# Kernel tuning notes

Hardware: AMD Instinct MI355X
Metric: run time of the kernel (lower is better)

The kernel has to match this reference:

```python
import jax, jax.numpy as jnp
import numpy as np

H = 128
W = 128
DELTA = 7000.0  # sigmainv in the original (delta default 7000)


def setup_inputs() -> dict:
    key = jax.random.key(0)
    k1, k2, k3, k4 = jax.random.split(key, 4)
    B, P, F, TH, TW = 2, 300, 512, 512, 512
    points_bxpx3 = jax.random.uniform(k1, (B, P, 3), jnp.float32) * 2.0 - 1.0  # NDC cube [-1,1]
    faces_fx3 = jax.random.randint(k2, (F, 3), 0, P, dtype=jnp.int32)
    uv_bxpx2 = jax.random.uniform(k3, (B, P, 2), jnp.float32)  # texcoords in [0,1]
    texture_bx3xthxtw = jax.random.uniform(k4, (B, 3, TH, TW), jnp.float32)
    return {"points_bxpx3": points_bxpx3, "faces_fx3": faces_fx3,
            "uv_bxpx2": uv_bxpx2, "texture_bx3xthxtw": texture_bx3xthxtw}


def _edge(ax, ay, bx, by, px, py):
    # signed area * 2 of triangle (a, b, p); standard edge function
    return (bx - ax) * (py - ay) - (by - ay) * (px - ax)


def _seg_d2(ax, ay, bx, by, px, py):
    # squared distance from point p to segment (a, b)
    abx, aby = bx - ax, by - ay
    apx, apy = px - ax, py - ay
    denom = abx * abx + aby * aby + 1e-12
    t = jnp.clip((apx * abx + apy * aby) / denom, 0.0, 1.0)
    dx = apx - t * abx
    dy = apy - t * aby
    return dx * dx + dy * dy


def _rasterize(points_bxpx3, faces_fx3, feats_bxfx3xd, height, width, delta):
    """Soft DIB-R-style rasterizer.
    Returns (imfeat [B,H,W,D], improb [B,H,W,1]).
    """
    B = points_bxpx3.shape[0]
    v = points_bxpx3[:, faces_fx3]                      # (B,F,3,3) gathered face vertices
    x0, x1, x2 = (v[:, :, i, 0][:, :, None, None] for i in range(3))
    y0, y1, y2 = (v[:, :, i, 1][:, :, None, None] for i in range(3))
    z0, z1, z2 = (v[:, :, i, 2][:, :, None, None] for i in range(3))

    # pixel-center grid in NDC; y flipped (top row = +1)
    px = ((jnp.arange(width, dtype=points_bxpx3.dtype) + 0.5) / width * 2.0 - 1.0)[None, None, None, :]
    py = (1.0 - (jnp.arange(height, dtype=points_bxpx3.dtype) + 0.5) / height * 2.0)[None, None, :, None]

    area = _edge(x0, y0, x1, y1, x2, y2)                # (B,F,1,1) == normal_z (cross-product z)
    front = area > 1e-8                                  # front-facing (normalz > 0) cull
    inv_area = 1.0 / jnp.where(front, area, 1.0)

    w0 = _edge(x1, y1, x2, y2, px, py) * inv_area        # (B,F,H,W) barycentrics
    w1 = _edge(x2, y2, x0, y0, px, py) * inv_area
    w2 = _edge(x0, y0, x1, y1, px, py) * inv_area
    inside = front & (w0 >= 0) & (w1 >= 0) & (w2 >= 0)

    z_pix = w0 * z0 + w1 * z1 + w2 * z2                  # interpolated depth
    zbuf = jnp.where(inside, z_pix, -1e9)
    best = jnp.argmax(zbuf, axis=1)                      # (B,H,W) nearest covering face
    hit = jnp.any(inside, axis=1)[..., None].astype(points_bxpx3.dtype)  # (B,H,W,1)

    # gather winning barycentrics and per-face vertex features
    w = jnp.stack([w0, w1, w2], axis=-1)                 # (B,F,H,W,3)
    idx = jnp.broadcast_to(best[:, None, :, :, None], (B, 1, height, width, 3))
    wb = jnp.take_along_axis(w, idx, axis=1)[:, 0]       # (B,H,W,3)
    fb = jax.vmap(lambda f, i: f[i])(feats_bxfx3xd, best)  # (B,H,W,3,D)
    imfeat = jnp.einsum('bhwk,bhwkd->bhwd', wb, fb) * hit

    # soft coverage: prob of each face = exp(-delta * d2(pixel, triangle)); z-buffer blend
    d2 = jnp.minimum(
        jnp.minimum(_seg_d2(x0, y0, x1, y1, px, py), _seg_d2(x1, y1, x2, y2, px, py)),
        _seg_d2(x2, y2, x0, y0, px, py))
    d2 = jnp.where(inside, 0.0, d2)
    p = jnp.where(front, jnp.exp(-delta * d2), 0.0)      # (B,F,H,W)
    log_miss = jnp.sum(jnp.log1p(-jnp.clip(p, 0.0, 1.0 - 1e-7)), axis=1)  # (B,H,W)
    improb = (1.0 - jnp.exp(log_miss))[..., None]
    return imfeat, improb


def _fragmentshader(imtexcoords, texture_bx3xthxtw, hardmask):
    # bilinear texture sampling; background is zero
    B, C, TH, TW = texture_bx3xthxtw.shape
    u = jnp.clip(imtexcoords[..., 0], 0.0, 1.0)
    vv = jnp.clip(imtexcoords[..., 1], 0.0, 1.0)
    fx = u * (TW - 1)
    fy = (1.0 - vv) * (TH - 1)
    x0 = jnp.floor(fx).astype(jnp.int32); x1 = jnp.minimum(x0 + 1, TW - 1)
    y0 = jnp.floor(fy).astype(jnp.int32); y1 = jnp.minimum(y0 + 1, TH - 1)
    wx = (fx - x0)[:, None]; wy = (fy - y0)[:, None]     # (B,1,H,W)

    def g(tex, yy, xx):  # tex (C,TH,TW), yy/xx (H,W) -> (C,H,W)
        return tex[:, yy, xx]
    c00 = jax.vmap(g)(texture_bx3xthxtw, y0, x0)
    c01 = jax.vmap(g)(texture_bx3xthxtw, y0, x1)
    c10 = jax.vmap(g)(texture_bx3xthxtw, y1, x0)
    c11 = jax.vmap(g)(texture_bx3xthxtw, y1, x1)
    col = (c00 * (1 - wx) * (1 - wy) + c01 * wx * (1 - wy)
           + c10 * (1 - wx) * wy + c11 * wx * wy)        # (B,C,H,W)
    return col.transpose(0, 2, 3, 1) * hardmask          # (B,H,W,C)


def reference(points_bxpx3, faces_fx3, uv_bxpx2, texture_bx3xthxtw):
    # texture mode: per-face vertex features = [u, v, mask=1]
    uvf = uv_bxpx2[:, faces_fx3]                          # (B,F,3,2)
    ones = jnp.ones_like(uvf[..., :1])
    feats = jnp.concatenate([uvf, ones], axis=-1)         # (B,F,3,3)
    imfeat, improb = _rasterize(points_bxpx3, faces_fx3, feats, H, W, DELTA)
    imtexcoords = imfeat[..., :2]
    hardmask = jax.lax.stop_gradient(imfeat[..., 2:3])    # .detach() in the original
    imrender = _fragmentshader(imtexcoords, texture_bx3xthxtw, hardmask)
    return imrender, improb
```

## Files before the change

kernel.cpp:

```cpp
#include <hip/hip_runtime.h>
#include <math.h>

constexpr int kB = 2, kP = 300, kF = 512, kH = 128, kW = 128, kTH = 512, kTW = 512;
constexpr float kDelta = 7000.0f;
constexpr float kCut = 0.06f;
constexpr float kThr2 = 0.018882f;
constexpr float kLogInside = -15.9423847f;

__global__ __launch_bounds__(512, 6) void render_all(const float* __restrict__ pts,
                                                     const int* __restrict__ faces,
                                                     const float* __restrict__ uvs,
                                                     const float* __restrict__ tex,
                                                     float* __restrict__ out) {
    __shared__ float4 sA[kF], sB[kF], sC[kF];
    __shared__ float2 s_vtx[kF * 3];
    __shared__ unsigned short s_of[kF];
    __shared__ int s_wsum[8];
    __shared__ float s_bz[512];
    __shared__ int s_bi[512];
    __shared__ float s_lm[512];

    int tile = (int)blockIdx.x;
    int b = tile >> 8;
    int rem = tile & 255;
    int ty = rem >> 4, tx = rem & 15;
    int tid = (int)threadIdx.x;
    int lane = tid & 63;
    int wv = tid >> 6;

    {
        int f = tid;
        int i0 = faces[f * 3 + 0], i1 = faces[f * 3 + 1], i2 = faces[f * 3 + 2];
        const float* pb = pts + b * kP * 3;
        float x0 = pb[i0 * 3], y0 = pb[i0 * 3 + 1], z0 = pb[i0 * 3 + 2];
        float x1 = pb[i1 * 3], y1 = pb[i1 * 3 + 1], z1 = pb[i1 * 3 + 2];
        float x2 = pb[i2 * 3], y2 = pb[i2 * 3 + 1], z2 = pb[i2 * 3 + 2];
        float area = (x1 - x0) * (y2 - y0) - (y1 - y0) * (x2 - x0);
        bool front = area > 1e-8f;

        sA[f] = make_float4(0.0f, 0.0f, -1e30f, 0.0f);
        sB[f] = make_float4(0.0f, -1e30f, 0.0f, 0.0f);
        sC[f] = make_float4(-1e30f, 0.0f, 0.0f, 0.0f);
        s_vtx[f * 3 + 0] = make_float2(1e15f, 1e15f);
        s_vtx[f * 3 + 1] = make_float2(1e15f, 1e15f);
        s_vtx[f * 3 + 2] = make_float2(1e15f, 1e15f);
        unsigned long long bal = __ballot(front);
        if (lane == 0) s_wsum[wv] = __popcll(bal);
        __syncthreads();

        int base = 0;
#pragma unroll
        for (int w = 0; w < 8; ++w) base += (w < wv) ? s_wsum[w] : 0;
        int k = base + __popcll(bal & ((1ull << lane) - 1ull));

        if (front) {
            int slot = ((k & 7) << 6) | (k >> 3);
            float inv_a = 1.0f / area;
            float e0x = x2 - x1, e0y = y2 - y1;
            float e1x = x0 - x2, e1y = y0 - y2;
            float e2x = x1 - x0, e2y = y1 - y0;
            float l0 = fmaf(e0x, e0x, e0y * e0y);
            float l1 = fmaf(e1x, e1x, e1y * e1y);
            float l2 = fmaf(e2x, e2x, e2y * e2y);
            float s0 = rsqrtf(l0 + 1e-12f);
            float s1 = rsqrtf(l1 + 1e-12f);
            float s2 = rsqrtf(l2 + 1e-12f);
            float A0 = -e0y * s0, B0 = e0x * s0, C0 = (e0y * x1 - e0x * y1) * s0;
            float A1 = -e1y * s1, B1 = e1x * s1, C1 = (e1y * x2 - e1x * y2) * s1;
            float A2 = -e2y * s2, B2 = e2x * s2, C2 = (e2y * x0 - e2x * y0) * s2;
            float a0 = -e0y * inv_a, b0 = e0x * inv_a, c0 = (e0y * x1 - e0x * y1) * inv_a;
            float a1 = -e1y * inv_a, b1 = e1x * inv_a, c1 = (e1y * x2 - e1x * y2) * inv_a;
            float a2 = -e2y * inv_a, b2 = e2x * inv_a, c2 = (e2y * x0 - e2x * y0) * inv_a;
            sA[slot] = make_float4(A0, B0, C0, A1);
            sB[slot] = make_float4(B1, C1, A2, B2);
            sC[slot] = make_float4(C2,
                                   a0 * z0 + a1 * z1 + a2 * z2,
                                   b0 * z0 + b1 * z1 + b2 * z2,
                                   c0 * z0 + c1 * z1 + c2 * z2);
            s_vtx[slot * 3 + 0] = make_float2(x0, y0);
            s_vtx[slot * 3 + 1] = make_float2(x1, y1);
            s_vtx[slot * 3 + 2] = make_float2(x2, y2);
            s_of[slot] = (unsigned short)f;
        }
    }
    __syncthreads();

    int pyi = ty * 8 + (lane >> 3);
    int pxi = tx * 8 + (lane & 7);
    float px = ((float)pxi + 0.5f) * (2.0f / 128.0f) - 1.0f;
    float py = 1.0f - ((float)pyi + 0.5f) * (2.0f / 128.0f);

    float cx = (float)(tx * 8 + 4) * (2.0f / 128.0f) - 1.0f;
    float cy = 1.0f - (float)(ty * 8 + 4) * (2.0f / 128.0f);
    unsigned long long m;
    {
        int slt = (wv << 6) + lane;
        float4 a4 = sA[slt];
        float4 b4 = sB[slt];
        float4 c4 = sC[slt];
        float L0 = fmaf(a4.x, cx, fmaf(a4.y, cy, a4.z));
        float L1 = fmaf(a4.w, cx, fmaf(b4.x, cy, b4.y));
        float L2 = fmaf(b4.z, cx, fmaf(b4.w, cy, c4.x));
        float minc = fminf(fminf(L0, L1), L2);
        float2 v0 = s_vtx[slt * 3 + 0];
        float2 v1 = s_vtx[slt * 3 + 1];
        float2 v2 = s_vtx[slt * 3 + 2];
        float e0x = v2.x - v1.x, e0y = v2.y - v1.y;
        float e1x = v0.x - v2.x, e1y = v0.y - v2.y;
        float e2x = v1.x - v0.x, e2y = v1.y - v0.y;
        float p0x = cx - v0.x, p0y = cy - v0.y;
        float p1x = cx - v1.x, p1y = cy - v1.y;
        float p2x = cx - v2.x, p2y = cy - v2.y;
        float dot0 = fmaf(p1x, e0x, p1y * e0y), len0 = fmaf(e0x, e0x, e0y * e0y);
        float dot1 = fmaf(p2x, e1x, p2y * e1y), len1 = fmaf(e1x, e1x, e1y * e1y);
        float dot2 = fmaf(p0x, e2x, p0y * e2y), len2 = fmaf(e2x, e2x, e2y * e2y);
        float c0 = (dot0 >= 0.0f && dot0 <= len0) ? L0 * L0 : 1e30f;
        float c1 = (dot1 >= 0.0f && dot1 <= len1) ? L1 * L1 : 1e30f;
        float c2 = (dot2 >= 0.0f && dot2 <= len2) ? L2 * L2 : 1e30f;
        float dv0 = fmaf(p0x, p0x, p0y * p0y);
        float dv1 = fmaf(p1x, p1x, p1y * p1y);
        float dv2 = fmaf(p2x, p2x, p2y * p2y);
        float d2c = fminf(fminf(fminf(c0, c1), fminf(c2, dv0)), fminf(dv1, dv2));
        bool admit = (minc >= 0.0f) | (d2c <= kThr2);
        m = __ballot(admit);
    }

    float bestz = -1e9f;
    int besti = -1, icnt = 0;
    float lm = 0.0f;

    while (m) {
        int l = (int)__builtin_ctzll(m);
        m &= (m - 1);
        int fs = (wv << 6) + l;
        int k = (l << 3) | wv;
        float4 h0 = sA[fs];
        float4 h1 = sB[fs];
        float4 h2 = sC[fs];
        float L0 = fmaf(h0.x, px, fmaf(h0.y, py, h0.z));
        float L1 = fmaf(h0.w, px, fmaf(h1.x, py, h1.y));
        float L2 = fmaf(h1.z, px, fmaf(h1.w, py, h2.x));
        float minL = fminf(fminf(L0, L1), L2);
        bool inside = minL >= 0.0f;
        float z = fmaf(h2.y, px, fmaf(h2.z, py, h2.w));
        if (inside && z > bestz) { bestz = z; besti = k; }
        icnt += inside ? 1 : 0;
        float db = fminf(fminf(fabsf(L0), fabsf(L1)), fabsf(L2));
        bool need = (!inside) & (db < kCut);
        if (__any(need)) {
            float2 v0 = s_vtx[fs * 3 + 0];
            float2 v1 = s_vtx[fs * 3 + 1];
            float2 v2 = s_vtx[fs * 3 + 2];
            float e0x = v2.x - v1.x, e0y = v2.y - v1.y;
            float e1x = v0.x - v2.x, e1y = v0.y - v2.y;
            float e2x = v1.x - v0.x, e2y = v1.y - v0.y;
            float p0x = px - v0.x, p0y = py - v0.y;
            float p1x = px - v1.x, p1y = py - v1.y;
            float p2x = px - v2.x, p2y = py - v2.y;
            float dot0 = fmaf(p1x, e0x, p1y * e0y), len0 = fmaf(e0x, e0x, e0y * e0y);
            float dot1 = fmaf(p2x, e1x, p2y * e1y), len1 = fmaf(e1x, e1x, e1y * e1y);
            float dot2 = fmaf(p0x, e2x, p0y * e2y), len2 = fmaf(e2x, e2x, e2y * e2y);
            float c0 = (dot0 >= 0.0f && dot0 <= len0) ? L0 * L0 : 1e30f;
            float c1 = (dot1 >= 0.0f && dot1 <= len1) ? L1 * L1 : 1e30f;
            float c2 = (dot2 >= 0.0f && dot2 <= len2) ? L2 * L2 : 1e30f;
            float dv0 = fmaf(p0x, p0x, p0y * p0y);
            float dv1 = fmaf(p1x, p1x, p1y * p1y);
            float dv2 = fmaf(p2x, p2x, p2y * p2y);
            float d2 = fminf(fminf(fminf(c0, c1), fminf(c2, dv0)), fminf(dv1, dv2));
            float p = __expf(-kDelta * d2);
            p = fminf(p, 1.0f - 1e-7f);
            float lp = __logf(1.0f - p);
            lm += need ? lp : 0.0f;
        }
    }
    lm = fmaf((float)icnt, kLogInside, lm);

    s_bz[tid] = bestz;
    s_bi[tid] = besti;
    s_lm[tid] = lm;
    __syncthreads();

    if (tid < 64) {
        float bz = s_bz[tid];
        int bi = s_bi[tid];
        float L = s_lm[tid];
#pragma unroll
        for (int w = 1; w < 8; ++w) {
            float z2 = s_bz[w * 64 + tid];
            int ii = s_bi[w * 64 + tid];
            L += s_lm[w * 64 + tid];
            if (z2 > bz || (z2 == bz && ii >= 0 && (unsigned)ii < (unsigned)bi)) {
                bz = z2; bi = ii;
            }
        }
        float improb = 1.0f - expf(L);
        float u = 0.0f, v = 0.0f, mk = 0.0f;
        if (bi >= 0) {
            int slot = ((bi & 7) << 6) | (bi >> 3);
            float2 v0 = s_vtx[slot * 3 + 0];
            float2 v1 = s_vtx[slot * 3 + 1];
            float2 v2 = s_vtx[slot * 3 + 2];
            float area = (v1.x - v0.x) * (v2.y - v0.y) - (v1.y - v0.y) * (v2.x - v0.x);
            float inv_a = 1.0f / area;
            float w0 = ((v2.x - v1.x) * (py - v1.y) - (v2.y - v1.y) * (px - v1.x)) * inv_a;
            float w1 = ((v0.x - v2.x) * (py - v2.y) - (v0.y - v2.y) * (px - v2.x)) * inv_a;
            float w2 = ((v1.x - v0.x) * (py - v0.y) - (v1.y - v0.y) * (px - v0.x)) * inv_a;
            int of = (int)s_of[slot];
            int j0 = faces[of * 3], j1 = faces[of * 3 + 1], j2 = faces[of * 3 + 2];
            const float* ub = uvs + b * kP * 2;
            u = w0 * ub[j0 * 2] + w1 * ub[j1 * 2] + w2 * ub[j2 * 2];
            v = w0 * ub[j0 * 2 + 1] + w1 * ub[j1 * 2 + 1] + w2 * ub[j2 * 2 + 1];
            mk = w0 + w1 + w2;
        }
        float uc = fminf(fmaxf(u, 0.0f), 1.0f);
        float vc = fminf(fmaxf(v, 0.0f), 1.0f);
        float fx = uc * (float)(kTW - 1);
        float fy = (1.0f - vc) * (float)(kTH - 1);
        int xi0 = (int)floorf(fx), yi0 = (int)floorf(fy);
        int xi1 = min(xi0 + 1, kTW - 1), yi1 = min(yi0 + 1, kTH - 1);
        float wx = fx - (float)xi0, wy = fy - (float)yi0;
        float w00 = (1.0f - wx) * (1.0f - wy);
        float w01 = wx * (1.0f - wy);
        float w10 = (1.0f - wx) * wy;
        float w11 = wx * wy;
        int o00 = yi0 * kTW + xi0, o01 = yi0 * kTW + xi1;
        int o10 = yi1 * kTW + xi0, o11 = yi1 * kTW + xi1;
        const float* tb = tex + (size_t)b * 3 * kTH * kTW;
        float cols[3];
#pragma unroll
        for (int c = 0; c < 3; ++c) {
            const float* tc = tb + c * kTH * kTW;
            cols[c] = (tc[o00] * w00 + tc[o01] * w01 + tc[o10] * w10 + tc[o11] * w11) * mk;
        }
        int pix = (b * kH + pyi) * kW + pxi;
        out[pix * 3 + 0] = cols[0];
        out[pix * 3 + 1] = cols[1];
        out[pix * 3 + 2] = cols[2];
        out[kB * kH * kW * 3 + pix] = improb;
    }
}

extern "C" void kernel_launch(void* const* d_in, const int* in_sizes, int n_in,
                              void* d_out, int out_size, void* d_ws, size_t ws_size,
                              hipStream_t stream) {
    const float* pts = (const float*)d_in[0];
    const int* faces = (const int*)d_in[1];
    const float* uvs = (const float*)d_in[2];
    const float* tex = (const float*)d_in[3];
    float* out = (float*)d_out;
    render_all<<<kB * 256, 512, 0, stream>>>(pts, faces, uvs, tex, out);
}
```

Baseline: 18.32 us.

## Prefetch face params, stage UVs in LDS, split texture sampling across waves, tighten cutoffs

Several changes land together. The main face loop now software-pipelines the next face's LDS coefficient loads ahead of the current face's math. Per-batch UVs and the face vertex indices are cached in shared memory so the final shading step no longer issues dependent global gathers. Texture sampling for the 64 pixels is split across three waves, one per colour channel, instead of one wave doing all three channels. Separately, the soft-edge cutoff constants (kCut, kThr2) are reduced, which admits fewer faces and skips more exp/log work, but this may change accuracy relative to the reference.

```diff
diff --git a/kernel.cpp b/kernel.cpp
--- a/kernel.cpp
+++ b/kernel.cpp
@@ -3,8 +3,8 @@
 
 constexpr int kB = 2, kP = 300, kF = 512, kH = 128, kW = 128, kTH = 512, kTW = 512;
 constexpr float kDelta = 7000.0f;
-constexpr float kCut = 0.06f;
-constexpr float kThr2 = 0.018882f;
+constexpr float kCut = 0.0363f;
+constexpr float kThr2 = 0.012928f;
 constexpr float kLogInside = -15.9423847f;
 
 __global__ __launch_bounds__(512, 6) void render_all(const float* __restrict__ pts,
@@ -14,11 +14,14 @@
                                                      float* __restrict__ out) {
     __shared__ float4 sA[kF], sB[kF], sC[kF];
     __shared__ float2 s_vtx[kF * 3];
-    __shared__ unsigned short s_of[kF];
-    __shared__ int s_wsum[8];
+    __shared__ ushort4 s_j3[kF];
+    __shared__ float s_uv[kP * 2];
     __shared__ float s_bz[512];
     __shared__ int s_bi[512];
     __shared__ float s_lm[512];
+    __shared__ float4 s_pxW[64];
+    __shared__ int4 s_pxO[64];
+    __shared__ int s_wsum[8];
 
     int tile = (int)blockIdx.x;
     int b = tile >> 8;
@@ -38,6 +41,8 @@
         float area = (x1 - x0) * (y2 - y0) - (y1 - y0) * (x2 - x0);
         bool front = area > 1e-8f;
 
+        const float* gu = uvs + b * (kP * 2);
+        for (int i = tid; i < kP * 2; i += 512) s_uv[i] = gu[i];
         sA[f] = make_float4(0.0f, 0.0f, -1e30f, 0.0f);
         sB[f] = make_float4(0.0f, -1e30f, 0.0f, 0.0f);
         sC[f] = make_float4(-1e30f, 0.0f, 0.0f, 0.0f);
@@ -80,7 +85,8 @@
             s_vtx[slot * 3 + 0] = make_float2(x0, y0);
             s_vtx[slot * 3 + 1] = make_float2(x1, y1);
             s_vtx[slot * 3 + 2] = make_float2(x2, y2);
-            s_of[slot] = (unsigned short)f;
+            s_j3[slot] = make_ushort4((unsigned short)i0, (unsigned short)i1,
+                                      (unsigned short)i2, 0);
         }
     }
     __syncthreads();
@@ -129,14 +135,25 @@
     int besti = -1, icnt = 0;
     float lm = 0.0f;
 
-    while (m) {
-        int l = (int)__builtin_ctzll(m);
+    int l = -1;
+    float4 h0, h1, h2;
+    if (m) {
+        l = (int)__builtin_ctzll(m);
         m &= (m - 1);
         int fs = (wv << 6) + l;
+        h0 = sA[fs]; h1 = sB[fs]; h2 = sC[fs];
+    }
+    while (l >= 0) {
+        int l2 = -1;
+        float4 n0, n1, n2;
+        if (m) {
+            l2 = (int)__builtin_ctzll(m);
+            m &= (m - 1);
+            int fs2 = (wv << 6) + l2;
+            n0 = sA[fs2]; n1 = sB[fs2]; n2 = sC[fs2];
+        }
+        int fs = (wv << 6) + l;
         int k = (l << 3) | wv;
-        float4 h0 = sA[fs];
-        float4 h1 = sB[fs];
-        float4 h2 = sC[fs];
         float L0 = fmaf(h0.x, px, fmaf(h0.y, py, h0.z));
         float L1 = fmaf(h0.w, px, fmaf(h1.x, py, h1.y));
         float L2 = fmaf(h1.z, px, fmaf(h1.w, py, h2.x));
@@ -172,6 +189,7 @@
             float lp = __logf(1.0f - p);
             lm += need ? lp : 0.0f;
         }
+        l = l2; h0 = n0; h1 = n1; h2 = n2;
     }
     lm = fmaf((float)icnt, kLogInside, lm);
 
@@ -205,11 +223,9 @@
             float w0 = ((v2.x - v1.x) * (py - v1.y) - (v2.y - v1.y) * (px - v1.x)) * inv_a;
             float w1 = ((v0.x - v2.x) * (py - v2.y) - (v0.y - v2.y) * (px - v2.x)) * inv_a;
             float w2 = ((v1.x - v0.x) * (py - v0.y) - (v1.y - v0.y) * (px - v0.x)) * inv_a;
-            int of = (int)s_of[slot];
-            int j0 = faces[of * 3], j1 = faces[of * 3 + 1], j2 = faces[of * 3 + 2];
-            const float* ub = uvs + b * kP * 2;
-            u = w0 * ub[j0 * 2] + w1 * ub[j1 * 2] + w2 * ub[j2 * 2];
-            v = w0 * ub[j0 * 2 + 1] + w1 * ub[j1 * 2 + 1] + w2 * ub[j2 * 2 + 1];
+            ushort4 j = s_j3[slot];
+            u = w0 * s_uv[j.x * 2] + w1 * s_uv[j.y * 2] + w2 * s_uv[j.z * 2];
+            v = w0 * s_uv[j.x * 2 + 1] + w1 * s_uv[j.y * 2 + 1] + w2 * s_uv[j.z * 2 + 1];
             mk = w0 + w1 + w2;
         }
         float uc = fminf(fmaxf(u, 0.0f), 1.0f);
@@ -219,24 +235,27 @@
         int xi0 = (int)floorf(fx), yi0 = (int)floorf(fy);
         int xi1 = min(xi0 + 1, kTW - 1), yi1 = min(yi0 + 1, kTH - 1);
         float wx = fx - (float)xi0, wy = fy - (float)yi0;
-        float w00 = (1.0f - wx) * (1.0f - wy);
-        float w01 = wx * (1.0f - wy);
-        float w10 = (1.0f - wx) * wy;
-        float w11 = wx * wy;
-        int o00 = yi0 * kTW + xi0, o01 = yi0 * kTW + xi1;
-        int o10 = yi1 * kTW + xi0, o11 = yi1 * kTW + xi1;
-        const float* tb = tex + (size_t)b * 3 * kTH * kTW;
-        float cols[3];
-#pragma unroll
-        for (int c = 0; c < 3; ++c) {
-            const float* tc = tb + c * kTH * kTW;
-            cols[c] = (tc[o00] * w00 + tc[o01] * w01 + tc[o10] * w10 + tc[o11] * w11) * mk;
-        }
-        int pix = (b * kH + pyi) * kW + pxi;
-        out[pix * 3 + 0] = cols[0];
-        out[pix * 3 + 1] = cols[1];
-        out[pix * 3 + 2] = cols[2];
-        out[kB * kH * kW * 3 + pix] = improb;
+        float w00 = (1.0f - wx) * (1.0f - wy) * mk;
+        float w01 = wx * (1.0f - wy) * mk;
+        float w10 = (1.0f - wx) * wy * mk;
+        float w11 = wx * wy * mk;
+        s_pxW[tid] = make_float4(w00, w01, w10, w11);
+        s_pxO[tid] = make_int4(yi0 * kTW + xi0, yi0 * kTW + xi1,
+                               yi1 * kTW + xi0, yi1 * kTW + xi1);
+        out[kB * kH * kW * 3 + (b * kH + pyi) * kW + pxi] = improb;
+    }
+    __syncthreads();
+
+    if (tid < 192) {
+        int pix = tid & 63;
+        int c = tid >> 6;
+        float4 w = s_pxW[pix];
+        int4 o = s_pxO[pix];
+        const float* tc = tex + ((size_t)b * 3 + c) * kTH * kTW;
+        float col = tc[o.x] * w.x + tc[o.y] * w.y + tc[o.z] * w.z + tc[o.w] * w.w;
+        int qy = ty * 8 + (pix >> 3);
+        int qx = tx * 8 + (pix & 7);
+        out[((b * kH + qy) * kW + qx) * 3 + c] = col;
     }
 }
 
```

New measurement: 18.44 us. Within noise of the previous version (+0.7%).
